# Optimization experiments

Measured on AMD Instinct MI355X. Metric: run time of the kernel, lower is better.

## Reference

```python
import jax, jax.numpy as jnp
import numpy as np

K = 5
PAD = K // 2
EPS = 1e-12  # F.normalize eps


def setup_inputs() -> dict:
    key = jax.random.key(0)
    k1, k2, k3 = jax.random.split(key, 3)
    b, c, h, w = 8, 1024, 64, 64
    out_ch = 1024
    feature = jax.random.normal(k1, (b, c, h, w), dtype=jnp.float32)
    # Conv2d(1024 + K*K, out_ch, 1) -> weight [out_ch, 1049], bias [out_ch]
    conv_w = jax.random.normal(k2, (out_ch, c + K * K), dtype=jnp.float32) * 0.02
    conv_b = jax.random.normal(k3, (out_ch,), dtype=jnp.float32) * 0.02
    return {"feature": feature, "conv_w": conv_w, "conv_b": conv_b}


def reference(feature, conv_w, conv_b):
    b, c, h, w = feature.shape
    # L2-normalize over channel dim (F.normalize: x / max(||x||, eps))
    norm = jnp.sqrt(jnp.sum(feature * feature, axis=1, keepdims=True))
    fn = feature / jnp.maximum(norm, EPS)
    fp = jnp.pad(fn, ((0, 0), (0, 0), (PAD, PAD), (PAD, PAD)))
    # 25 shifted correlations; order matches torch loop: index = col*K + row
    corr = jnp.stack(
        [jnp.sum(fp[:, :, r:h + r, cc:w + cc] * fn, axis=1)
         for cc in range(K) for r in range(K)],
        axis=1,
    )  # [b, K*K, h, w]
    cat = jnp.concatenate([feature, corr], axis=1)  # [b, c+K*K, h, w]
    y = jnp.einsum('oc,bchw->bohw', conv_w, cat) + conv_b[None, :, None, None]
    return jax.nn.relu(y)
```

## Files before the change

kernel.cpp:

```cpp
#include <hip/hip_runtime.h>
#include <hip/hip_bf16.h>


typedef __attribute__((ext_vector_type(8))) short short8x;
typedef __attribute__((ext_vector_type(4))) float floatx4;

#define B_   8
#define C_   1024
#define HW_  4096
#define KPAD 1088
#define NT   17

__device__ __forceinline__ unsigned short f2bf(float f) {
  unsigned int u = __float_as_uint(f);
  u += 0x7FFFu + ((u >> 16) & 1u);
  return (unsigned short)(u >> 16);
}

__device__ __forceinline__ void async16(const void* g, void* l) {
  __builtin_amdgcn_global_load_lds(
      (__attribute__((address_space(1))) void*)(void*)g,
      (__attribute__((address_space(3))) void*)l, 16, 0, 0);
}

__device__ __forceinline__ short8x rd16(const char* p) {
  return *(const short8x*)p;
}

__global__ __launch_bounds__(512) void scn_aux(
    const float* __restrict__ f, float* __restrict__ corr,
    unsigned short* __restrict__ At, const float* __restrict__ w,
    unsigned short* __restrict__ Wb) {
  __shared__ float lds2[2][64][65];
  const int n = blockIdx.x;
  const int tid = threadIdx.x;

  if (n >= 4608) {
    const int base = (n - 4608) * 4096 + tid * 8;
    const int o = base / KPAD, kk = base - o * KPAD;
    short8x v;
#pragma unroll
    for (int e = 0; e < 8; ++e) {
      const int k = kk + e;
      v[e] = (k < 1049) ? (short)f2bf(w[(size_t)o * 1049 + k]) : (short)0;
    }
    *(short8x*)(Wb + (size_t)o * KPAD + kk) = v;
    return;
  }

  const int g = n / 9, r = n - g * 9;
  if (r == 0) {
    const int x = tid & 63;
    const int y = (g & 7) * 8 + (tid >> 6);
    const int cs = (g >> 3) & 7, b = g >> 6;

    const int xs0 = (x + 2 < 64) ? x + 2 : 63;
    const int xs1 = (x + 1 < 64) ? x + 1 : 63;
    const int xs3 = (x - 1 >= 0) ? x - 1 : 0;
    const int xs4 = (x - 2 >= 0) ? x - 2 : 0;

    const bool ym2 = (y >= 2), ym1 = (y >= 1), yp1 = (y <= 62), yp2 = (y <= 61);

    const float* rp0 = f + ((size_t)b * C_ + cs * 128) * HW_ + y * 64;

    float h[25];
#pragma unroll
    for (int j = 0; j < 25; ++j) h[j] = 0.f;

#pragma unroll 4
    for (int c = 0; c < 128; ++c) {
      const float* rp = rp0 + (size_t)c * HW_;
      const float ctr = rp[x];
      const float vm2 = ym2 ? rp[x - 128] : 0.f;
      const float vm1 = ym1 ? rp[x - 64] : 0.f;
      const float vp1 = yp1 ? rp[x + 64] : 0.f;
      const float vp2 = yp2 ? rp[x + 128] : 0.f;
      const float c0 = __shfl(ctr, xs0, 64);
      const float c1 = __shfl(ctr, xs1, 64);
      const float c3 = __shfl(ctr, xs3, 64);
      const float c4 = __shfl(ctr, xs4, 64);
      const float v[5] = {vm2, vm1, ctr, vp1, vp2};
      const float cc[5] = {c0, c1, ctr, c3, c4};
#pragma unroll
      for (int dxi = 0; dxi < 5; ++dxi)
#pragma unroll
        for (int dyi = 0; dyi < 5; ++dyi)
          h[dxi * 5 + dyi] = fmaf(v[dyi], cc[dxi], h[dxi * 5 + dyi]);
    }

    float* pb = corr + b * HW_ + y * 64;
#pragma unroll
    for (int j = 0; j < 25; ++j) {
      const int dx = (j / 5) - 2;
      const int tgt = x - dx;
      const int wx = (tgt + 64) & 63;
      const float val = ((unsigned)tgt < 64u) ? h[j] : 0.f;
      atomicAdd(pb + (size_t)j * 32768 + wx, val);
    }
  } else {
    const int half = tid >> 8, t256 = tid & 255;
    const int tile = (g * 8 + (r - 1)) * 2 + half;
    const int b = tile >> 10, rem = tile & 1023;
    const int kt = rem >> 6, mt = rem & 63;

    const int m4 = (t256 & 15) << 2, kr0 = t256 >> 4;
    const float* src = f + ((size_t)b * C_ + kt * 64 + kr0) * HW_ + mt * 64 + m4;
#pragma unroll
    for (int i = 0; i < 4; ++i) {
      floatx4 v = *(const floatx4*)(src + (size_t)i * 16 * HW_);
      float* d = &lds2[half][kr0 + i * 16][m4];
      d[0] = v[0]; d[1] = v[1]; d[2] = v[2]; d[3] = v[3];
    }
    __syncthreads();
    unsigned short* dst = At + ((size_t)b * HW_ + mt * 64) * KPAD + kt * 64;
    const int c = t256 & 7, mr = t256 >> 3;
#pragma unroll
    for (int h2 = 0; h2 < 2; ++h2) {
      const int mm = mr + h2 * 32;
      short8x v;
#pragma unroll
      for (int j = 0; j < 8; ++j) v[j] = (short)f2bf(lds2[half][c * 8 + j][mm]);
      *(short8x*)(dst + (size_t)mm * KPAD + c * 8) = v;
    }
  }
}

__global__ __launch_bounds__(256) void scn_reduce2(
    const float* __restrict__ corr, unsigned short* __restrict__ At) {
  __shared__ float linv[8][64];
  const int b = blockIdx.y;
  const int bx = blockIdx.x;
  const int tid = threadIdx.x;
  const int x = tid & 63;
  const int y0 = bx * 4;

  const float* c12 = corr + (size_t)12 * 32768 + b * HW_;
#pragma unroll
  for (int rr = 0; rr < 2; ++rr) {
    const int rsel = (tid >> 6) + rr * 4;
    const int yy = y0 - 2 + rsel;
    const float s = (yy >= 0 && yy < 64) ? c12[yy * 64 + x] : 1.0f;
    linv[rsel][x] = 1.0f / fmaxf(sqrtf(s), 1e-12f);
  }
  __syncthreads();

  const int m = bx * 256 + tid;
  const int i = b * HW_ + m;
  const int yr = tid >> 6;
  const float ic = linv[yr + 2][x];

  unsigned short r[64];
#pragma unroll
  for (int j = 0; j < 25; ++j) {
    const float acc = corr[(size_t)j * 32768 + i];
    const int dy = (j % 5) - 2, dx = (j / 5) - 2;
    const int ny = y0 + yr + dy, nx = x + dx;
    const float in2 = (ny >= 0 && ny < 64 && nx >= 0 && nx < 64)
                          ? linv[yr + 2 + dy][nx] : 0.f;
    r[j] = f2bf(acc * ic * in2);
  }
#pragma unroll
  for (int j = 25; j < 64; ++j) r[j] = 0;
  unsigned short* row = At + ((size_t)b * HW_ + m) * KPAD + 1024;
#pragma unroll
  for (int v = 0; v < 8; ++v) *(short8x*)(row + v * 8) = *(short8x*)(r + v * 8);
}

__global__ __launch_bounds__(512, 2) void scn_gemm(
    const unsigned short* __restrict__ Wb, const unsigned short* __restrict__ At,
    const float* __restrict__ bias, float* __restrict__ out) {
  extern __shared__ char lds[];
  const int tid = threadIdx.x;
  const int l = tid & 63;
  const int wid = tid >> 6;
  const int wm = wid >> 2;
  const int wn = wid & 3;
  const int nb = blockIdx.x, ob = blockIdx.y, b = blockIdx.z;

  const int rr = tid >> 3;
  const int cswz = ((tid & 7) ^ (rr & 7)) << 3;
  const unsigned short* gA = Wb + (size_t)(ob * 256 + rr) * KPAD + cswz;
  const unsigned short* gB = At + ((size_t)b * HW_ + nb * 256 + rr) * KPAD + cswz;
  char* const dBase = (char*)lds + tid * 16;

#define ISSUE_A(bf, kt)                                         \
  do {                                                          \
    const unsigned short* _s = gA + (kt) * 64;                  \
    char* _d = dBase + (bf) * 65536;                            \
    async16(_s, _d);                                            \
    async16(_s + (size_t)64 * KPAD, _d + 8192);                 \
    async16(_s + (size_t)128 * KPAD, _d + 16384);               \
    async16(_s + (size_t)192 * KPAD, _d + 24576);               \
  } while (0)

#define ISSUE_B(bf, kt)                                         \
  do {                                                          \
    const unsigned short* _s = gB + (kt) * 64;                  \
    char* _d = dBase + (bf) * 65536 + 32768;                    \
    async16(_s, _d);                                            \
    async16(_s + (size_t)64 * KPAD, _d + 8192);                 \
    async16(_s + (size_t)128 * KPAD, _d + 16384);               \
    async16(_s + (size_t)192 * KPAD, _d + 24576);               \
  } while (0)

  const int l15 = l & 15, l4g = l >> 4, l7 = l & 7;
  const int aoff0 = l15 * 128 + ((l4g ^ l7) << 4);
  const int aoff1 = l15 * 128 + (((l4g + 4) ^ l7) << 4);
  const char* aB0 = (const char*)lds + wm * 16384;
  const char* bB0 = (const char*)lds + 32768 + (wn >> 1) * 16384 + (wn & 1) * 8192;

  floatx4 acc[8][4];
#pragma unroll
  for (int i = 0; i < 8; ++i)
#pragma unroll
    for (int j = 0; j < 4; ++j) acc[i][j] = (floatx4){0.f, 0.f, 0.f, 0.f};

  ISSUE_A(0, 0); ISSUE_B(0, 0);
  ISSUE_A(1, 1); ISSUE_B(1, 1);
  asm volatile("s_waitcnt vmcnt(8)" ::: "memory");
  __builtin_amdgcn_s_barrier();

  short8x a[4][2], b0[2][2], b1[2][2];

  for (int t = 0; t < NT; ++t) {
    const int bf = t & 1;
    const char* ab = aB0 + bf * 65536;
    const char* bb = bB0 + bf * 65536;
    const int t2 = (t < NT - 2) ? (t + 2) : 0;

#pragma unroll
    for (int i = 0; i < 4; ++i) {
      a[i][0] = rd16(ab + i * 2048 + aoff0);
      a[i][1] = rd16(ab + i * 2048 + aoff1);
    }
#pragma unroll
    for (int j = 0; j < 2; ++j) {
      b0[j][0] = rd16(bb + j * 2048 + aoff0);
      b0[j][1] = rd16(bb + j * 2048 + aoff1);
    }
    __builtin_amdgcn_s_barrier();
    asm volatile("s_waitcnt lgkmcnt(0)" ::: "memory");
    __builtin_amdgcn_sched_barrier(0);
    __builtin_amdgcn_s_setprio(1);
#pragma unroll
    for (int i = 0; i < 4; ++i)
#pragma unroll
      for (int j = 0; j < 2; ++j) {
        acc[i][j] = __builtin_amdgcn_mfma_f32_16x16x32_bf16(a[i][0], b0[j][0], acc[i][j], 0, 0, 0);
        acc[i][j] = __builtin_amdgcn_mfma_f32_16x16x32_bf16(a[i][1], b0[j][1], acc[i][j], 0, 0, 0);
      }
    __builtin_amdgcn_s_setprio(0);
    __builtin_amdgcn_s_barrier();

#pragma unroll
    for (int j = 0; j < 2; ++j) {
      b1[j][0] = rd16(bb + (2 + j) * 2048 + aoff0);
      b1[j][1] = rd16(bb + (2 + j) * 2048 + aoff1);
    }
    __builtin_amdgcn_s_barrier();
    asm volatile("s_waitcnt lgkmcnt(0)" ::: "memory");
    __builtin_amdgcn_sched_barrier(0);
    __builtin_amdgcn_s_setprio(1);
#pragma unroll
    for (int i = 0; i < 4; ++i)
#pragma unroll
      for (int j = 0; j < 2; ++j) {
        acc[i][2 + j] = __builtin_amdgcn_mfma_f32_16x16x32_bf16(a[i][0], b1[j][0], acc[i][2 + j], 0, 0, 0);
        acc[i][2 + j] = __builtin_amdgcn_mfma_f32_16x16x32_bf16(a[i][1], b1[j][1], acc[i][2 + j], 0, 0, 0);
      }
    __builtin_amdgcn_s_setprio(0);
    __builtin_amdgcn_s_barrier();

#pragma unroll
    for (int i = 0; i < 4; ++i) {
      a[i][0] = rd16(ab + (4 + i) * 2048 + aoff0);
      a[i][1] = rd16(ab + (4 + i) * 2048 + aoff1);
    }
    ISSUE_B(bf, t2);
    __builtin_amdgcn_s_barrier();
    asm volatile("s_waitcnt lgkmcnt(0)" ::: "memory");
    __builtin_amdgcn_sched_barrier(0);
    __builtin_amdgcn_s_setprio(1);
#pragma unroll
    for (int i = 0; i < 4; ++i)
#pragma unroll
      for (int j = 0; j < 2; ++j) {
        acc[4 + i][2 + j] = __builtin_amdgcn_mfma_f32_16x16x32_bf16(a[i][0], b1[j][0], acc[4 + i][2 + j], 0, 0, 0);
        acc[4 + i][2 + j] = __builtin_amdgcn_mfma_f32_16x16x32_bf16(a[i][1], b1[j][1], acc[4 + i][2 + j], 0, 0, 0);
      }
    __builtin_amdgcn_s_setprio(0);
    __builtin_amdgcn_s_barrier();

    ISSUE_A(bf, t2);
    __builtin_amdgcn_s_barrier();
    __builtin_amdgcn_s_setprio(1);
#pragma unroll
    for (int i = 0; i < 4; ++i)
#pragma unroll
      for (int j = 0; j < 2; ++j) {
        acc[4 + i][j] = __builtin_amdgcn_mfma_f32_16x16x32_bf16(a[i][0], b0[j][0], acc[4 + i][j], 0, 0, 0);
        acc[4 + i][j] = __builtin_amdgcn_mfma_f32_16x16x32_bf16(a[i][1], b0[j][1], acc[4 + i][j], 0, 0, 0);
      }
    __builtin_amdgcn_s_setprio(0);
    asm volatile("s_waitcnt vmcnt(8)" ::: "memory");
    __builtin_amdgcn_s_barrier();
  }
  asm volatile("s_waitcnt vmcnt(0)" ::: "memory");
#undef ISSUE_A
#undef ISSUE_B

  float* outb = out + (size_t)b * C_ * HW_;
#pragma unroll
  for (int i = 0; i < 8; ++i) {
    const int o0 = ob * 256 + wm * 128 + i * 16 + l4g * 4;
    float bs[4];
#pragma unroll
    for (int r = 0; r < 4; ++r) bs[r] = bias[o0 + r];
#pragma unroll
    for (int j = 0; j < 4; ++j) {
      const int m = nb * 256 + wn * 64 + j * 16 + l15;
#pragma unroll
      for (int r = 0; r < 4; ++r) {
        float v = acc[i][j][r] + bs[r];
        outb[(size_t)(o0 + r) * HW_ + m] = v > 0.f ? v : 0.f;
      }
    }
  }
}

extern "C" void kernel_launch(void* const* d_in, const int* in_sizes, int n_in,
                              void* d_out, int out_size, void* d_ws, size_t ws_size,
                              hipStream_t stream) {
  const float* feature = (const float*)d_in[0];
  const float* conv_w  = (const float*)d_in[1];
  const float* conv_b  = (const float*)d_in[2];
  float* out = (float*)d_out;

  char* ws = (char*)d_ws;
  unsigned short* At = (unsigned short*)(ws);
  float* corr        = (float*)(ws + 71303168);
  unsigned short* Wb = (unsigned short*)(ws + 74579968);

  static int gemm_attr_set = 0;
  if (!gemm_attr_set) {
    hipFuncSetAttribute((const void*)scn_gemm,
                        hipFuncAttributeMaxDynamicSharedMemorySize, 131072);
    gemm_attr_set = 1;
  }

  hipMemsetAsync(corr, 0, 25 * 32768 * sizeof(float), stream);
  scn_aux<<<dim3(4880), 512, 0, stream>>>(feature, corr, At, conv_w, Wb);
  scn_reduce2<<<dim3(16, 8), 256, 0, stream>>>(corr, At);
  scn_gemm<<<dim3(16, 4, 8), 512, 131072, stream>>>(Wb, At, conv_b, out);
}
```

Baseline: 379.0 us.

## Fuse correlation partials into transpose tiles sharing LDS-staged feature rows

The separate correlation blocks, which streamed 128 channels per row from global memory, are removed. Each transpose tile (64 channels × one image row) now computes partial 25-tap correlations too, reusing the center row already staged in LDS for the bf16 transpose and loading only the four neighbouring rows from global. Per-block partials are first reduced in LDS with shared atomics and then flushed to global with atomicAdd. This reads the feature tensor once instead of twice, but it raises global atomic traffic, with 16 channel-chunk partials per output instead of 8, and adds shared-memory atomics and more blocks.

```diff
diff --git a/kernel.cpp b/kernel.cpp
--- a/kernel.cpp
+++ b/kernel.cpp
@@ -10,6 +10,7 @@
 #define HW_  4096
 #define KPAD 1088
 #define NT   17
+#define NWC  272
 
 __device__ __forceinline__ unsigned short f2bf(float f) {
   unsigned int u = __float_as_uint(f);
@@ -31,12 +32,13 @@
     const float* __restrict__ f, float* __restrict__ corr,
     unsigned short* __restrict__ At, const float* __restrict__ w,
     unsigned short* __restrict__ Wb) {
-  __shared__ float lds2[2][64][65];
+  __shared__ float lds2[64][65];
+  __shared__ float rbuf[25][64];
   const int n = blockIdx.x;
   const int tid = threadIdx.x;
 
-  if (n >= 4608) {
-    const int base = (n - 4608) * 4096 + tid * 8;
+  if (n < NWC) {
+    const int base = n * 4096 + tid * 8;
     const int o = base / KPAD, kk = base - o * KPAD;
     short8x v;
 #pragma unroll
@@ -48,79 +50,86 @@
     return;
   }
 
-  const int g = n / 9, r = n - g * 9;
-  if (r == 0) {
-    const int x = tid & 63;
-    const int y = (g & 7) * 8 + (tid >> 6);
-    const int cs = (g >> 3) & 7, b = g >> 6;
-
-    const int xs0 = (x + 2 < 64) ? x + 2 : 63;
-    const int xs1 = (x + 1 < 64) ? x + 1 : 63;
-    const int xs3 = (x - 1 >= 0) ? x - 1 : 0;
-    const int xs4 = (x - 2 >= 0) ? x - 2 : 0;
-
-    const bool ym2 = (y >= 2), ym1 = (y >= 1), yp1 = (y <= 62), yp2 = (y <= 61);
-
-    const float* rp0 = f + ((size_t)b * C_ + cs * 128) * HW_ + y * 64;
-
-    float h[25];
-#pragma unroll
-    for (int j = 0; j < 25; ++j) h[j] = 0.f;
-
-#pragma unroll 4
-    for (int c = 0; c < 128; ++c) {
-      const float* rp = rp0 + (size_t)c * HW_;
-      const float ctr = rp[x];
-      const float vm2 = ym2 ? rp[x - 128] : 0.f;
-      const float vm1 = ym1 ? rp[x - 64] : 0.f;
-      const float vp1 = yp1 ? rp[x + 64] : 0.f;
-      const float vp2 = yp2 ? rp[x + 128] : 0.f;
-      const float c0 = __shfl(ctr, xs0, 64);
-      const float c1 = __shfl(ctr, xs1, 64);
-      const float c3 = __shfl(ctr, xs3, 64);
-      const float c4 = __shfl(ctr, xs4, 64);
-      const float v[5] = {vm2, vm1, ctr, vp1, vp2};
-      const float cc[5] = {c0, c1, ctr, c3, c4};
-#pragma unroll
-      for (int dxi = 0; dxi < 5; ++dxi)
-#pragma unroll
-        for (int dyi = 0; dyi < 5; ++dyi)
-          h[dxi * 5 + dyi] = fmaf(v[dyi], cc[dxi], h[dxi * 5 + dyi]);
-    }
-
-    float* pb = corr + b * HW_ + y * 64;
-#pragma unroll
-    for (int j = 0; j < 25; ++j) {
+  const int t = n - NWC;
+  const int mt = t & 63;
+  const int kt = (t >> 6) & 15;
+  const int b  = t >> 10;
+  const int y  = mt;
+
+#pragma unroll
+  for (int z = tid; z < 1600; z += 512) ((float*)rbuf)[z] = 0.f;
+
+  const int m4 = (tid & 15) << 2, kr0 = tid >> 4;
+  const float* src = f + ((size_t)b * C_ + kt * 64 + kr0) * HW_ + y * 64 + m4;
+#pragma unroll
+  for (int i = 0; i < 2; ++i) {
+    floatx4 v = *(const floatx4*)(src + (size_t)i * 32 * HW_);
+    float* d = &lds2[kr0 + i * 32][m4];
+    d[0] = v[0]; d[1] = v[1]; d[2] = v[2]; d[3] = v[3];
+  }
+
+  const int x = tid & 63, g = tid >> 6;
+  const bool ym2 = (y >= 2), ym1 = (y >= 1), yp1 = (y <= 62), yp2 = (y <= 61);
+  const float* fbase = f + ((size_t)b * C_ + kt * 64 + g * 8) * HW_ + y * 64 + x;
+  float vm2[8], vm1[8], vp1[8], vp2[8];
+#pragma unroll
+  for (int cc = 0; cc < 8; ++cc) {
+    const float* rp = fbase + (size_t)cc * HW_;
+    vm2[cc] = ym2 ? rp[-128] : 0.f;
+    vm1[cc] = ym1 ? rp[-64] : 0.f;
+    vp1[cc] = yp1 ? rp[64] : 0.f;
+    vp2[cc] = yp2 ? rp[128] : 0.f;
+  }
+
+  __syncthreads();
+
+  {
+    const int c = tid & 7, mr = tid >> 3;
+    unsigned short* dst =
+        At + ((size_t)b * HW_ + mt * 64 + mr) * KPAD + kt * 64 + c * 8;
+    short8x v;
+#pragma unroll
+    for (int j = 0; j < 8; ++j) v[j] = (short)f2bf(lds2[c * 8 + j][mr]);
+    *(short8x*)dst = v;
+  }
+
+  const int xs0 = (x + 2 < 64) ? x + 2 : 63;
+  const int xs1 = (x + 1 < 64) ? x + 1 : 63;
+  const int xs3 = (x - 1 >= 0) ? x - 1 : 0;
+  const int xs4 = (x - 2 >= 0) ? x - 2 : 0;
+
+  float h[25];
+#pragma unroll
+  for (int j = 0; j < 25; ++j) h[j] = 0.f;
+#pragma unroll
+  for (int cc = 0; cc < 8; ++cc) {
+    const float* lr = &lds2[g * 8 + cc][0];
+    const float ctr = lr[x];
+    const float c0 = lr[xs0], c1 = lr[xs1], c3 = lr[xs3], c4 = lr[xs4];
+    const float v[5] = {vm2[cc], vm1[cc], ctr, vp1[cc], vp2[cc]};
+    const float ccv[5] = {c0, c1, ctr, c3, c4};
+#pragma unroll
+    for (int dxi = 0; dxi < 5; ++dxi)
+#pragma unroll
+      for (int dyi = 0; dyi < 5; ++dyi)
+        h[dxi * 5 + dyi] = fmaf(v[dyi], ccv[dxi], h[dxi * 5 + dyi]);
+  }
+
+#pragma unroll
+  for (int j = 0; j < 25; ++j) atomicAdd(&rbuf[j][x], h[j]);
+
+  __syncthreads();
+
+  float* cb = corr + b * HW_ + y * 64;
+#pragma unroll
+  for (int k = 0; k < 4; ++k) {
+    const int v = tid + k * 512;
+    if (v < 1600) {
+      const int j = v >> 6, xx = v & 63;
       const int dx = (j / 5) - 2;
-      const int tgt = x - dx;
-      const int wx = (tgt + 64) & 63;
-      const float val = ((unsigned)tgt < 64u) ? h[j] : 0.f;
-      atomicAdd(pb + (size_t)j * 32768 + wx, val);
-    }
-  } else {
-    const int half = tid >> 8, t256 = tid & 255;
-    const int tile = (g * 8 + (r - 1)) * 2 + half;
-    const int b = tile >> 10, rem = tile & 1023;
-    const int kt = rem >> 6, mt = rem & 63;
-
-    const int m4 = (t256 & 15) << 2, kr0 = t256 >> 4;
-    const float* src = f + ((size_t)b * C_ + kt * 64 + kr0) * HW_ + mt * 64 + m4;
-#pragma unroll
-    for (int i = 0; i < 4; ++i) {
-      floatx4 v = *(const floatx4*)(src + (size_t)i * 16 * HW_);
-      float* d = &lds2[half][kr0 + i * 16][m4];
-      d[0] = v[0]; d[1] = v[1]; d[2] = v[2]; d[3] = v[3];
-    }
-    __syncthreads();
-    unsigned short* dst = At + ((size_t)b * HW_ + mt * 64) * KPAD + kt * 64;
-    const int c = t256 & 7, mr = t256 >> 3;
-#pragma unroll
-    for (int h2 = 0; h2 < 2; ++h2) {
-      const int mm = mr + h2 * 32;
-      short8x v;
-#pragma unroll
-      for (int j = 0; j < 8; ++j) v[j] = (short)f2bf(lds2[half][c * 8 + j][mm]);
-      *(short8x*)(dst + (size_t)mm * KPAD + c * 8) = v;
+      const int tgt = xx - dx;
+      if ((unsigned)tgt < 64u)
+        atomicAdd(cb + (size_t)j * 32768 + tgt, ((float*)rbuf)[v]);
     }
   }
 }
@@ -349,7 +358,7 @@
   }
 
   hipMemsetAsync(corr, 0, 25 * 32768 * sizeof(float), stream);
-  scn_aux<<<dim3(4880), 512, 0, stream>>>(feature, corr, At, conv_w, Wb);
+  scn_aux<<<dim3(8464), 512, 0, stream>>>(feature, corr, At, conv_w, Wb);
   scn_reduce2<<<dim3(16, 8), 256, 0, stream>>>(corr, At);
   scn_gemm<<<dim3(16, 4, 8), 512, 131072, stream>>>(Wb, At, conv_b, out);
 }
```

New measurement: 812.0 us. +114.3%, slower.
